# Performance work log

Hardware: AMD Instinct MI355X
Metric: run time of the kernel (lower is better)

## Reference

```python
import jax, jax.numpy as jnp
import numpy as np

D_MODEL = 1024
NUM_HEADS = 16
HEAD_DIM = D_MODEL // NUM_HEADS
D_FF = 4096
LN_EPS = 1e-6  # flax nnx.LayerNorm default


def setup_inputs() -> dict:
    key = jax.random.key(0)
    ks = jax.random.split(key, 13)
    s_in = 1.0 / np.sqrt(D_MODEL)
    s_ff = 1.0 / np.sqrt(D_FF)
    return {
        "x": jax.random.normal(ks[0], (2, 2048, D_MODEL), dtype=jnp.float32),
        "Wq": jax.random.normal(ks[1], (D_MODEL, D_MODEL), jnp.float32) * s_in,
        "bq": jnp.zeros((D_MODEL,), jnp.float32),
        "Wk": jax.random.normal(ks[2], (D_MODEL, D_MODEL), jnp.float32) * s_in,
        "bk": jnp.zeros((D_MODEL,), jnp.float32),
        "Wv": jax.random.normal(ks[3], (D_MODEL, D_MODEL), jnp.float32) * s_in,
        "bv": jnp.zeros((D_MODEL,), jnp.float32),
        "Wo": jax.random.normal(ks[4], (D_MODEL, D_MODEL), jnp.float32) * s_in,
        "bo": jnp.zeros((D_MODEL,), jnp.float32),
        "W1": jax.random.normal(ks[5], (D_MODEL, D_FF), jnp.float32) * s_in,
        "b1": jnp.zeros((D_FF,), jnp.float32),
        "W2": jax.random.normal(ks[6], (D_FF, D_MODEL), jnp.float32) * s_ff,
        "b2": jnp.zeros((D_MODEL,), jnp.float32),
        "ln1_scale": jnp.ones((D_MODEL,), jnp.float32),
        "ln1_bias": jnp.zeros((D_MODEL,), jnp.float32),
        "ln2_scale": jnp.ones((D_MODEL,), jnp.float32),
        "ln2_bias": jnp.zeros((D_MODEL,), jnp.float32),
    }


def layer_norm(x, scale, bias):
    mu = jnp.mean(x, axis=-1, keepdims=True)
    var = jnp.mean(jnp.square(x - mu), axis=-1, keepdims=True)
    return (x - mu) * jax.lax.rsqrt(var + LN_EPS) * scale + bias


def reference(x, Wq, bq, Wk, bk, Wv, bv, Wo, bo, W1, b1, W2, b2,
              ln1_scale, ln1_bias, ln2_scale, ln2_bias):
    B, S, _ = x.shape
    h = layer_norm(x, ln1_scale, ln1_bias)
    # project and split heads: [B, H, S, Dh]
    q = (h @ Wq + bq).reshape(B, S, NUM_HEADS, HEAD_DIM).transpose(0, 2, 1, 3)
    k = (h @ Wk + bk).reshape(B, S, NUM_HEADS, HEAD_DIM).transpose(0, 2, 1, 3)
    v = (h @ Wv + bv).reshape(B, S, NUM_HEADS, HEAD_DIM).transpose(0, 2, 1, 3)
    scores = jnp.einsum("bhqd,bhkd->bhqk", q, k) / jnp.sqrt(jnp.float32(HEAD_DIM))
    attn = jax.nn.softmax(scores, axis=-1)
    out = jnp.einsum("bhqk,bhkd->bhqd", attn, v)
    out = out.transpose(0, 2, 1, 3).reshape(B, S, D_MODEL)
    x = x + out @ Wo + bo
    h2 = layer_norm(x, ln2_scale, ln2_bias)
    ff = jax.nn.relu(h2 @ W1 + b1) @ W2 + b2
    return x + ff
```

## Files before the change

### kernel.cpp

```cpp
#include <hip/hip_runtime.h>

typedef unsigned short ushort_t;
typedef __attribute__((ext_vector_type(8))) __bf16 bf16x8;
typedef __attribute__((ext_vector_type(4))) __bf16 bf16x4;
typedef __attribute__((ext_vector_type(8))) unsigned short ushort8v;
typedef __attribute__((ext_vector_type(4))) float floatx4;

__device__ inline float b2f(ushort_t u) {
    union { unsigned int i; float f; } c; c.i = ((unsigned int)u) << 16; return c.f;
}
__device__ inline ushort_t f2b(float f) {
    union { float f; unsigned int i; } c; c.f = f;
    unsigned int i = c.i;
    unsigned int r = (i + 0x7FFFu + ((i >> 16) & 1u)) >> 16;
    return (ushort_t)r;
}
__device__ inline bf16x8 as_bf16x8(ushort8v u) { return __builtin_bit_cast(bf16x8, u); }

__device__ inline void load_lds16(const ushort_t* g, ushort_t* l) {
    __builtin_amdgcn_global_load_lds(
        (const __attribute__((address_space(1))) void*)g,
        (__attribute__((address_space(3))) void*)l, 16, 0, 0);
}

__global__ __launch_bounds__(256) void concat3_kernel(
    const float* __restrict__ a, const float* __restrict__ b,
    const float* __restrict__ c, float* __restrict__ o) {
    int t = blockIdx.x * 256 + threadIdx.x;
    if (t < 3072)
        o[t] = t < 1024 ? a[t] : (t < 2048 ? b[t - 1024] : c[t - 2048]);
}

__global__ __launch_bounds__(256) void copy_f32_kernel(
    const float* __restrict__ src, float* __restrict__ dst) {
    size_t i = ((size_t)blockIdx.x * 256 + threadIdx.x) * 4;
    *(float4*)(dst + i) = *(const float4*)(src + i);
}

__global__ __launch_bounds__(256) void transpose_all_kernel(
    const float* __restrict__ Wq, const float* __restrict__ Wk,
    const float* __restrict__ Wv, const float* __restrict__ Wo,
    const float* __restrict__ W1, const float* __restrict__ W2,
    ushort_t* __restrict__ dq, ushort_t* __restrict__ dk,
    ushort_t* __restrict__ dv, ushort_t* __restrict__ do_,
    ushort_t* __restrict__ d1, ushort_t* __restrict__ d2) {
    int t = blockIdx.x;
    const float* src; ushort_t* dst; int R, ld, tcx, tcy;
    if (t < 4096) {
        int id = t >> 10, u = t & 1023;
        tcx = u & 31; tcy = u >> 5; R = 1024; ld = 1024;
        src = id == 0 ? Wq : id == 1 ? Wk : id == 2 ? Wv : Wo;
        dst = id == 0 ? dq : id == 1 ? dk : id == 2 ? dv : do_;
    } else if (t < 8192) {
        int u = t - 4096;
        tcx = u & 127; tcy = u >> 7; R = 1024; ld = 4096;
        src = W1; dst = d1;
    } else {
        int u = t - 8192;
        tcx = u & 31; tcy = u >> 5; R = 4096; ld = 1024;
        src = W2; dst = d2;
    }
    __shared__ float tile[32][33];
    int tx = threadIdx.x, ty = threadIdx.y;
    int r0 = tcy * 32, c0 = tcx * 32;
#pragma unroll
    for (int i = 0; i < 32; i += 8)
        tile[ty + i][tx] = src[(size_t)(r0 + ty + i) * ld + c0 + tx];
    __syncthreads();
#pragma unroll
    for (int i = 0; i < 32; i += 8)
        dst[(size_t)(c0 + ty + i) * R + r0 + tx] = f2b(tile[tx][ty + i]);
}

__global__ __launch_bounds__(256) void transpose_v_kernel(
    const ushort_t* __restrict__ qkv, ushort_t* __restrict__ vt) {
    __shared__ ushort_t tile[32][33];
    int tx = threadIdx.x, ty = threadIdx.y;
    int s0 = blockIdx.x * 32, d0 = blockIdx.y * 32;
    int bh = blockIdx.z, b = bh >> 4, h = bh & 15;
    const ushort_t* src = qkv + (size_t)b * 2048 * 3072 + 2048 + h * 64;
    ushort_t* dst = vt + (size_t)bh * 64 * 2048;
#pragma unroll
    for (int i = 0; i < 32; i += 8)
        tile[ty + i][tx] = src[(size_t)(s0 + ty + i) * 3072 + d0 + tx];
    __syncthreads();
#pragma unroll
    for (int i = 0; i < 32; i += 8)
        dst[(size_t)(d0 + ty + i) * 2048 + s0 + tx] = tile[tx][ty + i];
}

__device__ inline float wave_sum(float s) {
#pragma unroll
    for (int o = 32; o > 0; o >>= 1) s += __shfl_xor(s, o);
    return s;
}

__global__ __launch_bounds__(256) void ln_f32_kernel(
    const float* __restrict__ x, const float* __restrict__ sc,
    const float* __restrict__ bi, ushort_t* __restrict__ out) {
    int row = blockIdx.x, t = threadIdx.x;
    const float* xr = x + (size_t)row * 1024;
    float4 u = *(const float4*)(xr + t * 4);
    float v0 = u.x, v1 = u.y, v2 = u.z, v3 = u.w;
    __shared__ float sm[8];
    int wv = t >> 6, lane = t & 63;
    float s = wave_sum(v0 + v1 + v2 + v3);
    if (lane == 0) sm[wv] = s;
    __syncthreads();
    float mean = (sm[0] + sm[1] + sm[2] + sm[3]) * (1.0f / 1024.0f);
    float d0 = v0 - mean, d1 = v1 - mean, d2 = v2 - mean, d3 = v3 - mean;
    float q = wave_sum(d0 * d0 + d1 * d1 + d2 * d2 + d3 * d3);
    if (lane == 0) sm[4 + wv] = q;
    __syncthreads();
    float var = (sm[4] + sm[5] + sm[6] + sm[7]) * (1.0f / 1024.0f);
    float rn = rsqrtf(var + 1e-6f);
    float4 us = *(const float4*)(sc + t * 4);
    float4 ub = *(const float4*)(bi + t * 4);
    ushort4 o;
    o.x = f2b(d0 * rn * us.x + ub.x);
    o.y = f2b(d1 * rn * us.y + ub.y);
    o.z = f2b(d2 * rn * us.z + ub.z);
    o.w = f2b(d3 * rn * us.w + ub.w);
    *(ushort4*)(out + (size_t)row * 1024 + t * 4) = o;
}

__global__ __launch_bounds__(256) void gemm_bt_kernel(
    const ushort_t* __restrict__ A, const ushort_t* __restrict__ Bt,
    const float* __restrict__ bias, const float* __restrict__ resf,
    ushort_t* __restrict__ Cb, float* __restrict__ Cf,
    int M, int N, int K, int ldb, int op) {
    __shared__ __align__(16) ushort_t As[2][128 * 32];
    __shared__ __align__(16) ushort_t Bs[2][128 * 32];
    int tid = threadIdx.x;
    int m0 = blockIdx.y * 128, n0 = blockIdx.x * 128;
    int wv = tid >> 6, lane = tid & 63;
    int wr = wv & 1, wc = wv >> 1;
    int mo = wr * 64, no = wc * 64;
    int quad = lane >> 4, l16 = lane & 15;
    int k8 = quad * 8;

    floatx4 acc[4][4] = {};

    int e0 = tid * 8, e1 = 2048 + tid * 8;
    int r0 = e0 >> 5, kk0 = e0 & 31;
    int r1 = e1 >> 5, kk1 = e1 & 31;
    int wb0 = wv * 512, wb1 = 2048 + wv * 512;

    load_lds16(A + (size_t)(m0 + r0) * K + kk0, As[0] + wb0);
    load_lds16(Bt + (size_t)(n0 + r0) * ldb + kk0, Bs[0] + wb0);
    load_lds16(A + (size_t)(m0 + r1) * K + kk1, As[0] + wb1);
    load_lds16(Bt + (size_t)(n0 + r1) * ldb + kk1, Bs[0] + wb1);

    int buf = 0;
    for (int k0 = 0; k0 < K; k0 += 32) {
        __syncthreads();
        int nk = k0 + 32;
        if (nk < K) {
            int nb = buf ^ 1;
            load_lds16(A + (size_t)(m0 + r0) * K + nk + kk0, As[nb] + wb0);
            load_lds16(Bt + (size_t)(n0 + r0) * ldb + nk + kk0, Bs[nb] + wb0);
            load_lds16(A + (size_t)(m0 + r1) * K + nk + kk1, As[nb] + wb1);
            load_lds16(Bt + (size_t)(n0 + r1) * ldb + nk + kk1, Bs[nb] + wb1);
        }
        bf16x8 af[4], bfr[4];
#pragma unroll
        for (int i = 0; i < 4; ++i) {
            af[i]  = as_bf16x8(*(const ushort8v*)(As[buf] + (mo + i * 16 + l16) * 32 + k8));
            bfr[i] = as_bf16x8(*(const ushort8v*)(Bs[buf] + (no + i * 16 + l16) * 32 + k8));
        }
#pragma unroll
        for (int mi = 0; mi < 4; ++mi)
#pragma unroll
            for (int ni = 0; ni < 4; ++ni)
                acc[mi][ni] = __builtin_amdgcn_mfma_f32_16x16x32_bf16(
                    af[mi], bfr[ni], acc[mi][ni], 0, 0, 0);
        buf ^= 1;
    }

#pragma unroll
    for (int mi = 0; mi < 4; ++mi) {
#pragma unroll
        for (int r = 0; r < 4; ++r) {
            int row = m0 + mo + mi * 16 + quad * 4 + r;
            size_t rowoff = (size_t)row * N;
#pragma unroll
            for (int ni = 0; ni < 4; ++ni) {
                int col = n0 + no + ni * 16 + l16;
                float val = acc[mi][ni][r];
                if (op != 3) val += bias[col];
                if (op == 1) val = fmaxf(val, 0.0f);
                if (op >= 2) {
                    val += resf[rowoff + col];
                    Cf[rowoff + col] = val;
                } else {
                    Cb[rowoff + col] = f2b(val);
                }
            }
        }
    }
}

__global__ __launch_bounds__(256) void gemm_bt_atomic_kernel(
    const ushort_t* __restrict__ A, const ushort_t* __restrict__ Bt,
    const float* __restrict__ bias, float* __restrict__ Cf,
    int M, int N, int lda, int ldb, int Kc) {
    __shared__ __align__(16) ushort_t As[2][128 * 32];
    __shared__ __align__(16) ushort_t Bs[2][128 * 32];
    int tid = threadIdx.x;
    int m0 = blockIdx.y * 128, n0 = blockIdx.x * 128;
    int kbase = blockIdx.z * Kc;
    int wv = tid >> 6, lane = tid & 63;
    int wr = wv & 1, wc = wv >> 1;
    int mo = wr * 64, no = wc * 64;
    int quad = lane >> 4, l16 = lane & 15;
    int k8 = quad * 8;

    floatx4 acc[4][4] = {};

    int e0 = tid * 8, e1 = 2048 + tid * 8;
    int r0 = e0 >> 5, kk0 = e0 & 31;
    int r1 = e1 >> 5, kk1 = e1 & 31;
    int wb0 = wv * 512, wb1 = 2048 + wv * 512;

    load_lds16(A + (size_t)(m0 + r0) * lda + kbase + kk0, As[0] + wb0);
    load_lds16(Bt + (size_t)(n0 + r0) * ldb + kbase + kk0, Bs[0] + wb0);
    load_lds16(A + (size_t)(m0 + r1) * lda + kbase + kk1, As[0] + wb1);
    load_lds16(Bt + (size_t)(n0 + r1) * ldb + kbase + kk1, Bs[0] + wb1);

    int buf = 0;
    for (int k0 = kbase; k0 < kbase + Kc; k0 += 32) {
        __syncthreads();
        int nk = k0 + 32;
        if (nk < kbase + Kc) {
            int nb = buf ^ 1;
            load_lds16(A + (size_t)(m0 + r0) * lda + nk + kk0, As[nb] + wb0);
            load_lds16(Bt + (size_t)(n0 + r0) * ldb + nk + kk0, Bs[nb] + wb0);
            load_lds16(A + (size_t)(m0 + r1) * lda + nk + kk1, As[nb] + wb1);
            load_lds16(Bt + (size_t)(n0 + r1) * ldb + nk + kk1, Bs[nb] + wb1);
        }
        bf16x8 af[4], bfr[4];
#pragma unroll
        for (int i = 0; i < 4; ++i) {
            af[i]  = as_bf16x8(*(const ushort8v*)(As[buf] + (mo + i * 16 + l16) * 32 + k8));
            bfr[i] = as_bf16x8(*(const ushort8v*)(Bs[buf] + (no + i * 16 + l16) * 32 + k8));
        }
#pragma unroll
        for (int mi = 0; mi < 4; ++mi)
#pragma unroll
            for (int ni = 0; ni < 4; ++ni)
                acc[mi][ni] = __builtin_amdgcn_mfma_f32_16x16x32_bf16(
                    af[mi], bfr[ni], acc[mi][ni], 0, 0, 0);
        buf ^= 1;
    }

    bool addb = (blockIdx.z == 0) && (bias != nullptr);
#pragma unroll
    for (int mi = 0; mi < 4; ++mi) {
#pragma unroll
        for (int r = 0; r < 4; ++r) {
            int row = m0 + mo + mi * 16 + quad * 4 + r;
            size_t rowoff = (size_t)row * N;
#pragma unroll
            for (int ni = 0; ni < 4; ++ni) {
                int col = n0 + no + ni * 16 + l16;
                float val = acc[mi][ni][r];
                if (addb) val += bias[col];
                unsafeAtomicAdd(&Cf[rowoff + col], val);
            }
        }
    }
}

__global__ __launch_bounds__(256) void attn_kernel(
    const ushort_t* __restrict__ qkv, const ushort_t* __restrict__ vt,
    ushort_t* __restrict__ om) {
    const int LDQ = 3072, LDO = 1024;
    int bh = blockIdx.y;
    int b = bh >> 4, h = bh & 15;
    size_t qbase = (size_t)b * 2048 * LDQ + h * 64;
    size_t kbase = qbase + 1024;
    const ushort_t* vtp = vt + (size_t)bh * 64 * 2048;
    int q0 = blockIdx.x * 128;
    int tid = threadIdx.x, wv = tid >> 6, lane = tid & 63;
    int quad = lane >> 4, l16 = lane & 15;
    int k8 = quad * 8;

    __shared__ __align__(16) ushort_t Ks[64 * 72];
    __shared__ __align__(16) ushort_t Vs[64 * 72];
    __shared__ __align__(16) ushort_t Ps[4 * 32 * 76];
    ushort_t* ps = Ps + wv * 32 * 76;

    int sr0 = tid >> 3, scc0 = (tid & 7) * 8;
    int sr1 = sr0 + 32;

    bf16x8 qf[2][2];
#pragma unroll
    for (int mt = 0; mt < 2; ++mt) {
        const ushort_t* qptr = qkv + qbase + (size_t)(q0 + wv * 32 + mt * 16 + l16) * LDQ;
        qf[mt][0] = as_bf16x8(*(const ushort8v*)(qptr + k8));
        qf[mt][1] = as_bf16x8(*(const ushort8v*)(qptr + 32 + k8));
    }

    bf16x8 ones;
#pragma unroll
    for (int j = 0; j < 8; ++j) ones[j] = (__bf16)1.0f;

    floatx4 Oacc[2][4] = {};
    floatx4 lsum[2] = {};

    ushort8v kreg0, kreg1, vreg0, vreg1;
    kreg0 = *(const ushort8v*)(qkv + kbase + (size_t)sr0 * LDQ + scc0);
    kreg1 = *(const ushort8v*)(qkv + kbase + (size_t)sr1 * LDQ + scc0);
    vreg0 = *(const ushort8v*)(vtp + (size_t)sr0 * 2048 + scc0);
    vreg1 = *(const ushort8v*)(vtp + (size_t)sr1 * 2048 + scc0);

    for (int kb = 0; kb < 2048; kb += 64) {
        __syncthreads();
        *(ushort8v*)(Ks + sr0 * 72 + scc0) = kreg0;
        *(ushort8v*)(Ks + sr1 * 72 + scc0) = kreg1;
        *(ushort8v*)(Vs + sr0 * 72 + scc0) = vreg0;
        *(ushort8v*)(Vs + sr1 * 72 + scc0) = vreg1;
        __syncthreads();

        int nkb = (kb + 64 < 2048) ? kb + 64 : 0;
        kreg0 = *(const ushort8v*)(qkv + kbase + (size_t)(nkb + sr0) * LDQ + scc0);
        kreg1 = *(const ushort8v*)(qkv + kbase + (size_t)(nkb + sr1) * LDQ + scc0);
        vreg0 = *(const ushort8v*)(vtp + (size_t)sr0 * 2048 + nkb + scc0);
        vreg1 = *(const ushort8v*)(vtp + (size_t)sr1 * 2048 + nkb + scc0);

        bf16x8 kf[4][2];
#pragma unroll
        for (int kt = 0; kt < 4; ++kt)
#pragma unroll
            for (int ds = 0; ds < 2; ++ds)
                kf[kt][ds] = as_bf16x8(
                    *(const ushort8v*)(Ks + (kt * 16 + l16) * 72 + ds * 32 + k8));

        floatx4 sc[2][4];
#pragma unroll
        for (int mt = 0; mt < 2; ++mt)
#pragma unroll
            for (int kt = 0; kt < 4; ++kt) {
                floatx4 s = {0.0f, 0.0f, 0.0f, 0.0f};
                s = __builtin_amdgcn_mfma_f32_16x16x32_bf16(kf[kt][0], qf[mt][0], s, 0, 0, 0);
                s = __builtin_amdgcn_mfma_f32_16x16x32_bf16(kf[kt][1], qf[mt][1], s, 0, 0, 0);
                sc[mt][kt] = s;
            }

#pragma unroll
        for (int mt = 0; mt < 2; ++mt)
#pragma unroll
            for (int kt = 0; kt < 4; ++kt) {
                bf16x4 pb;
                pb[0] = (__bf16)__expf(sc[mt][kt][0] * 0.125f);
                pb[1] = (__bf16)__expf(sc[mt][kt][1] * 0.125f);
                pb[2] = (__bf16)__expf(sc[mt][kt][2] * 0.125f);
                pb[3] = (__bf16)__expf(sc[mt][kt][3] * 0.125f);
                *(bf16x4*)(ps + (mt * 16 + l16) * 76 + kt * 16 + quad * 4) = pb;
            }

        bf16x8 vf[4][2];
#pragma unroll
        for (int dt = 0; dt < 4; ++dt)
#pragma unroll
            for (int ks = 0; ks < 2; ++ks)
                vf[dt][ks] = as_bf16x8(
                    *(const ushort8v*)(Vs + (dt * 16 + l16) * 72 + ks * 32 + k8));
#pragma unroll
        for (int mt = 0; mt < 2; ++mt) {
            bf16x8 pf0 = as_bf16x8(*(const ushort8v*)(ps + (mt * 16 + l16) * 76 + k8));
            bf16x8 pf1 = as_bf16x8(*(const ushort8v*)(ps + (mt * 16 + l16) * 76 + 32 + k8));
#pragma unroll
            for (int dt = 0; dt < 4; ++dt) {
                Oacc[mt][dt] = __builtin_amdgcn_mfma_f32_16x16x32_bf16(pf0, vf[dt][0], Oacc[mt][dt], 0, 0, 0);
                Oacc[mt][dt] = __builtin_amdgcn_mfma_f32_16x16x32_bf16(pf1, vf[dt][1], Oacc[mt][dt], 0, 0, 0);
            }
            lsum[mt] = __builtin_amdgcn_mfma_f32_16x16x32_bf16(pf0, ones, lsum[mt], 0, 0, 0);
            lsum[mt] = __builtin_amdgcn_mfma_f32_16x16x32_bf16(pf1, ones, lsum[mt], 0, 0, 0);
        }
    }

#pragma unroll
    for (int mt = 0; mt < 2; ++mt)
#pragma unroll
        for (int r = 0; r < 4; ++r) {
            float inv = 1.0f / lsum[mt][r];
            size_t rowoff = (size_t)(b * 2048 + q0 + wv * 32 + mt * 16 + quad * 4 + r) * LDO + h * 64;
#pragma unroll
            for (int dt = 0; dt < 4; ++dt)
                om[rowoff + dt * 16 + l16] = f2b(Oacc[mt][dt][r] * inv);
        }
}

extern "C" void kernel_launch(void* const* d_in, const int* in_sizes, int n_in,
                              void* d_out, int out_size, void* d_ws, size_t ws_size,
                              hipStream_t stream) {
    const float* x    = (const float*)d_in[0];
    const float* Wq   = (const float*)d_in[1];
    const float* bq   = (const float*)d_in[2];
    const float* Wk   = (const float*)d_in[3];
    const float* bk   = (const float*)d_in[4];
    const float* Wv   = (const float*)d_in[5];
    const float* bv   = (const float*)d_in[6];
    const float* Wo   = (const float*)d_in[7];
    const float* bo   = (const float*)d_in[8];
    const float* W1   = (const float*)d_in[9];
    const float* b1   = (const float*)d_in[10];
    const float* W2   = (const float*)d_in[11];
    const float* b2   = (const float*)d_in[12];
    const float* ln1s = (const float*)d_in[13];
    const float* ln1b = (const float*)d_in[14];
    const float* ln2s = (const float*)d_in[15];
    const float* ln2b = (const float*)d_in[16];
    float*    outf = (float*)d_out;
    ushort_t* ws   = (ushort_t*)d_ws;

    const size_t M1 = 1048576;
    ushort_t* qkvT    = ws;
    ushort_t* WoT     = ws + 3 * M1;
    ushort_t* W1T     = ws + 4 * M1;
    ushort_t* W2T     = ws + 8 * M1;
    ushort_t* h       = ws + 12 * M1;
    ushort_t* attnout = ws + 12 * M1;
    ushort_t* qkv     = ws + 16 * M1;
    ushort_t* h2      = ws;
    ushort_t* ffbuf   = ws + 12 * M1;
    float*    bqkv    = (float*)d_out;
    ushort_t* vtbuf   = (ushort_t*)d_out;

    dim3 tb(32, 8);

    concat3_kernel<<<12, 256, 0, stream>>>(bq, bk, bv, bqkv);
    transpose_all_kernel<<<12288, tb, 0, stream>>>(
        Wq, Wk, Wv, Wo, W1, W2,
        qkvT, qkvT + M1, qkvT + 2 * M1, WoT, W1T, W2T);

    ln_f32_kernel<<<4096, 256, 0, stream>>>(x, ln1s, ln1b, h);

    gemm_bt_kernel<<<dim3(24, 32), 256, 0, stream>>>(
        h, qkvT, bqkv, nullptr, qkv, nullptr, 4096, 3072, 1024, 1024, 0);

    transpose_v_kernel<<<dim3(64, 2, 32), tb, 0, stream>>>(qkv, vtbuf);

    attn_kernel<<<dim3(16, 32), 256, 0, stream>>>(qkv, vtbuf, attnout);

    copy_f32_kernel<<<4096, 256, 0, stream>>>(x, outf);
    gemm_bt_atomic_kernel<<<dim3(8, 32, 4), 256, 0, stream>>>(
        attnout, WoT, bo, outf, 4096, 1024, 1024, 1024, 256);

    ln_f32_kernel<<<4096, 256, 0, stream>>>(outf, ln2s, ln2b, h2);

    gemm_bt_kernel<<<dim3(32, 32), 256, 0, stream>>>(
        h2, W1T, b1, nullptr, ffbuf, nullptr, 4096, 4096, 1024, 1024, 1);

    gemm_bt_atomic_kernel<<<dim3(8, 32, 4), 256, 0, stream>>>(
        ffbuf, W2T, b2, outf, 4096, 1024, 4096, 4096, 1024);
}
```

Baseline: 494.4 us.

## Triple-buffer GEMM LDS tiles with explicit vmcnt waits for deeper prefetch

Both bf16 GEMM kernels move from double to triple LDS buffering and prefetch two k-tiles ahead. Explicit s_waitcnt vmcnt counters plus a raw s_barrier replace __syncthreads, so the load for tile i+2 can still be in flight while tile i is computed. This is meant to hide more global-load latency. In exchange LDS use per block grows from 32KB to 48KB, which may lower occupancy, and the hand-written wait counts depend on the compiler not reordering other vector memory ops.

```diff
diff --git a/kernel.cpp b/kernel.cpp
--- a/kernel.cpp
+++ b/kernel.cpp
@@ -129,8 +129,8 @@
     const float* __restrict__ bias, const float* __restrict__ resf,
     ushort_t* __restrict__ Cb, float* __restrict__ Cf,
     int M, int N, int K, int ldb, int op) {
-    __shared__ __align__(16) ushort_t As[2][128 * 32];
-    __shared__ __align__(16) ushort_t Bs[2][128 * 32];
+    __shared__ __align__(16) ushort_t As[3][128 * 32];
+    __shared__ __align__(16) ushort_t Bs[3][128 * 32];
     int tid = threadIdx.x;
     int m0 = blockIdx.y * 128, n0 = blockIdx.x * 128;
     int wv = tid >> 6, lane = tid & 63;
@@ -145,28 +145,43 @@
     int r0 = e0 >> 5, kk0 = e0 & 31;
     int r1 = e1 >> 5, kk1 = e1 & 31;
     int wb0 = wv * 512, wb1 = 2048 + wv * 512;
-
-    load_lds16(A + (size_t)(m0 + r0) * K + kk0, As[0] + wb0);
-    load_lds16(Bt + (size_t)(n0 + r0) * ldb + kk0, Bs[0] + wb0);
-    load_lds16(A + (size_t)(m0 + r1) * K + kk1, As[0] + wb1);
-    load_lds16(Bt + (size_t)(n0 + r1) * ldb + kk1, Bs[0] + wb1);
-
-    int buf = 0;
-    for (int k0 = 0; k0 < K; k0 += 32) {
-        __syncthreads();
-        int nk = k0 + 32;
-        if (nk < K) {
-            int nb = buf ^ 1;
-            load_lds16(A + (size_t)(m0 + r0) * K + nk + kk0, As[nb] + wb0);
-            load_lds16(Bt + (size_t)(n0 + r0) * ldb + nk + kk0, Bs[nb] + wb0);
-            load_lds16(A + (size_t)(m0 + r1) * K + nk + kk1, As[nb] + wb1);
-            load_lds16(Bt + (size_t)(n0 + r1) * ldb + nk + kk1, Bs[nb] + wb1);
-        }
+    const ushort_t* Ar0 = A + (size_t)(m0 + r0) * K + kk0;
+    const ushort_t* Ar1 = A + (size_t)(m0 + r1) * K + kk1;
+    const ushort_t* Br0 = Bt + (size_t)(n0 + r0) * ldb + kk0;
+    const ushort_t* Br1 = Bt + (size_t)(n0 + r1) * ldb + kk1;
+
+    int niter = K >> 5;
+    load_lds16(Ar0, As[0] + wb0);
+    load_lds16(Br0, Bs[0] + wb0);
+    load_lds16(Ar1, As[0] + wb1);
+    load_lds16(Br1, Bs[0] + wb1);
+    load_lds16(Ar0 + 32, As[1] + wb0);
+    load_lds16(Br0 + 32, Bs[1] + wb0);
+    load_lds16(Ar1 + 32, As[1] + wb1);
+    load_lds16(Br1 + 32, Bs[1] + wb1);
+
+    for (int i = 0; i < niter; ++i) {
+        if (i < niter - 1)
+            __asm__ volatile("s_waitcnt vmcnt(4)" ::: "memory");
+        else
+            __asm__ volatile("s_waitcnt vmcnt(0)" ::: "memory");
+        __builtin_amdgcn_s_barrier();
+        __asm__ volatile("" ::: "memory");
+        if (i + 2 < niter) {
+            int nb = (i + 2) % 3;
+            int off = (i + 2) * 32;
+            load_lds16(Ar0 + off, As[nb] + wb0);
+            load_lds16(Br0 + off, Bs[nb] + wb0);
+            load_lds16(Ar1 + off, As[nb] + wb1);
+            load_lds16(Br1 + off, Bs[nb] + wb1);
+        }
+        const ushort_t* as = As[i % 3];
+        const ushort_t* bs = Bs[i % 3];
         bf16x8 af[4], bfr[4];
 #pragma unroll
-        for (int i = 0; i < 4; ++i) {
-            af[i]  = as_bf16x8(*(const ushort8v*)(As[buf] + (mo + i * 16 + l16) * 32 + k8));
-            bfr[i] = as_bf16x8(*(const ushort8v*)(Bs[buf] + (no + i * 16 + l16) * 32 + k8));
+        for (int j = 0; j < 4; ++j) {
+            af[j]  = as_bf16x8(*(const ushort8v*)(as + (mo + j * 16 + l16) * 32 + k8));
+            bfr[j] = as_bf16x8(*(const ushort8v*)(bs + (no + j * 16 + l16) * 32 + k8));
         }
 #pragma unroll
         for (int mi = 0; mi < 4; ++mi)
@@ -174,7 +189,6 @@
             for (int ni = 0; ni < 4; ++ni)
                 acc[mi][ni] = __builtin_amdgcn_mfma_f32_16x16x32_bf16(
                     af[mi], bfr[ni], acc[mi][ni], 0, 0, 0);
-        buf ^= 1;
     }
 
 #pragma unroll
@@ -204,8 +218,8 @@
     const ushort_t* __restrict__ A, const ushort_t* __restrict__ Bt,
     const float* __restrict__ bias, float* __restrict__ Cf,
     int M, int N, int lda, int ldb, int Kc) {
-    __shared__ __align__(16) ushort_t As[2][128 * 32];
-    __shared__ __align__(16) ushort_t Bs[2][128 * 32];
+    __shared__ __align__(16) ushort_t As[3][128 * 32];
+    __shared__ __align__(16) ushort_t Bs[3][128 * 32];
     int tid = threadIdx.x;
     int m0 = blockIdx.y * 128, n0 = blockIdx.x * 128;
     int kbase = blockIdx.z * Kc;
@@ -221,28 +235,43 @@
     int r0 = e0 >> 5, kk0 = e0 & 31;
     int r1 = e1 >> 5, kk1 = e1 & 31;
     int wb0 = wv * 512, wb1 = 2048 + wv * 512;
-
-    load_lds16(A + (size_t)(m0 + r0) * lda + kbase + kk0, As[0] + wb0);
-    load_lds16(Bt + (size_t)(n0 + r0) * ldb + kbase + kk0, Bs[0] + wb0);
-    load_lds16(A + (size_t)(m0 + r1) * lda + kbase + kk1, As[0] + wb1);
-    load_lds16(Bt + (size_t)(n0 + r1) * ldb + kbase + kk1, Bs[0] + wb1);
-
-    int buf = 0;
-    for (int k0 = kbase; k0 < kbase + Kc; k0 += 32) {
-        __syncthreads();
-        int nk = k0 + 32;
-        if (nk < kbase + Kc) {
-            int nb = buf ^ 1;
-            load_lds16(A + (size_t)(m0 + r0) * lda + nk + kk0, As[nb] + wb0);
-            load_lds16(Bt + (size_t)(n0 + r0) * ldb + nk + kk0, Bs[nb] + wb0);
-            load_lds16(A + (size_t)(m0 + r1) * lda + nk + kk1, As[nb] + wb1);
-            load_lds16(Bt + (size_t)(n0 + r1) * ldb + nk + kk1, Bs[nb] + wb1);
-        }
+    const ushort_t* Ar0 = A + (size_t)(m0 + r0) * lda + kbase + kk0;
+    const ushort_t* Ar1 = A + (size_t)(m0 + r1) * lda + kbase + kk1;
+    const ushort_t* Br0 = Bt + (size_t)(n0 + r0) * ldb + kbase + kk0;
+    const ushort_t* Br1 = Bt + (size_t)(n0 + r1) * ldb + kbase + kk1;
+
+    int niter = Kc >> 5;
+    load_lds16(Ar0, As[0] + wb0);
+    load_lds16(Br0, Bs[0] + wb0);
+    load_lds16(Ar1, As[0] + wb1);
+    load_lds16(Br1, Bs[0] + wb1);
+    load_lds16(Ar0 + 32, As[1] + wb0);
+    load_lds16(Br0 + 32, Bs[1] + wb0);
+    load_lds16(Ar1 + 32, As[1] + wb1);
+    load_lds16(Br1 + 32, Bs[1] + wb1);
+
+    for (int i = 0; i < niter; ++i) {
+        if (i < niter - 1)
+            __asm__ volatile("s_waitcnt vmcnt(4)" ::: "memory");
+        else
+            __asm__ volatile("s_waitcnt vmcnt(0)" ::: "memory");
+        __builtin_amdgcn_s_barrier();
+        __asm__ volatile("" ::: "memory");
+        if (i + 2 < niter) {
+            int nb = (i + 2) % 3;
+            int off = (i + 2) * 32;
+            load_lds16(Ar0 + off, As[nb] + wb0);
+            load_lds16(Br0 + off, Bs[nb] + wb0);
+            load_lds16(Ar1 + off, As[nb] + wb1);
+            load_lds16(Br1 + off, Bs[nb] + wb1);
+        }
+        const ushort_t* as = As[i % 3];
+        const ushort_t* bs = Bs[i % 3];
         bf16x8 af[4], bfr[4];
 #pragma unroll
-        for (int i = 0; i < 4; ++i) {
-            af[i]  = as_bf16x8(*(const ushort8v*)(As[buf] + (mo + i * 16 + l16) * 32 + k8));
-            bfr[i] = as_bf16x8(*(const ushort8v*)(Bs[buf] + (no + i * 16 + l16) * 32 + k8));
+        for (int j = 0; j < 4; ++j) {
+            af[j]  = as_bf16x8(*(const ushort8v*)(as + (mo + j * 16 + l16) * 32 + k8));
+            bfr[j] = as_bf16x8(*(const ushort8v*)(bs + (no + j * 16 + l16) * 32 + k8));
         }
 #pragma unroll
         for (int mi = 0; mi < 4; ++mi)
@@ -250,7 +279,6 @@
             for (int ni = 0; ni < 4; ++ni)
                 acc[mi][ni] = __builtin_amdgcn_mfma_f32_16x16x32_bf16(
                     af[mi], bfr[ni], acc[mi][ni], 0, 0, 0);
-        buf ^= 1;
     }
 
     bool addb = (blockIdx.z == 0) && (bias != nullptr);
```

Result: no change. 498.8 us (+0.9%).
